# Kernel optimization log

Measured on AMD Instinct MI355X. Metric: run time of the kernel, lower is better.

Reference implementation:

```python
import jax, jax.numpy as jnp
import numpy as np

K = 128
NITER = 10


def _sq_dist(x, c):
    x2 = jnp.sum(x * x, axis=1, keepdims=True)          # [N,1]
    c2 = jnp.sum(c * c, axis=1)                          # [K]
    return x2 + c2[None, :] - 2.0 * (x @ c.T)


def _kmeans(x, key):
    N, D = x.shape
    idx = jax.random.permutation(key, N)[:K]             # torch.randperm(N)[:K]
    c0 = x[idx]

    def step(c, _):
        cl = jnp.argmin(_sq_dist(x, c), axis=1)          # nearest assignment [N]
        counts = jax.ops.segment_sum(jnp.ones((N,), x.dtype), cl, num_segments=K)  # bincount
        sums = jax.ops.segment_sum(x, cl, num_segments=K)                          # [K,D] (vectorized over D)
        # c = sums / counts; NaN (empty cluster, 0/0) -> 0, matching c[isnan(c)]=0
        c_new = jnp.where(counts[:, None] > 0, sums / jnp.maximum(counts, 1.0)[:, None], 0.0)
        return c_new, None

    c, _ = jax.lax.scan(step, c0, None, length=NITER)
    return c


def setup_inputs() -> dict:
    key = jax.random.key(0)
    x = jax.random.normal(key, (500000, 64), dtype=jnp.float32)
    return {"x": x}


def reference(x):
    # KMeans runs on x.detach(); forward output has no grad path through centroids
    centroids = _kmeans(jax.lax.stop_gradient(x), jax.random.key(42))
    distances = _sq_dist(x, centroids)                   # [N, K]
    # Faithful to normalize_distance: distances.sum(1, keepdim=True)[0] indexes
    # ROW 0 of the [N,1] row-sums -> a single scalar broadcast to all rows.
    denom = jnp.sum(distances[0])
    probs = 1.0 - distances / denom
    return probs
```

## Files before the change

kernel.cpp:

```cpp
#include <hip/hip_runtime.h>
#include <cstdint>
#include <cstddef>

#define NPTS 500000
#define DIM 64
#define KC 128
#define KM_ITERS 10
#define NGROUPS (NPTS / 32)
#define NITERS8 ((NGROUPS + 7) / 8)

typedef __bf16 bf16x8 __attribute__((ext_vector_type(8)));
typedef float f32x4 __attribute__((ext_vector_type(4)));

__device__ __forceinline__ float wave_reduce_add(float v) {
#pragma unroll
  for (int off = 32; off > 0; off >>= 1) v += __shfl_xor(v, off, 64);
  return v;
}

__device__ __forceinline__ bf16x8 cvt8(float4 a, float4 b) {
  bf16x8 r;
  r[0] = (__bf16)a.x; r[1] = (__bf16)a.y; r[2] = (__bf16)a.z; r[3] = (__bf16)a.w;
  r[4] = (__bf16)b.x; r[5] = (__bf16)b.y; r[6] = (__bf16)b.z; r[7] = (__bf16)b.w;
  return r;
}

__global__ void k_cvt(const float* __restrict__ x, bf16x8* __restrict__ xb8) {
  int n = NPTS * DIM / 8;
  for (int i = blockIdx.x * 256 + threadIdx.x; i < n; i += gridDim.x * 256) {
    const float4* xp = (const float4*)(x + (size_t)i * 8);
    xb8[i] = cvt8(xp[0], xp[1]);
  }
}

__global__ void k_initc(const float* __restrict__ x, float* __restrict__ cent,
                        float* __restrict__ c2, float* __restrict__ sums,
                        float* __restrict__ cnts) {
  int k = blockIdx.x, d = threadIdx.x;
  long src = (long)k * 3891 + 7;
  float v = x[src * DIM + d];
  cent[k * DIM + d] = v;
  sums[k * DIM + d] = 0.f;
  float s = wave_reduce_add(v * v);
  if (d == 0) { c2[k] = s; cnts[k] = 0.f; }
}

__global__ void k_update(const float* __restrict__ sums, const float* __restrict__ cnts,
                         float* __restrict__ cent, float* __restrict__ c2,
                         float* __restrict__ sums_z, float* __restrict__ cnts_z) {
  int k = blockIdx.x, d = threadIdx.x;
  float c = cnts[k];
  float v = (c > 0.f) ? (sums[k * DIM + d] / c) : 0.f;
  cent[k * DIM + d] = v;
  sums_z[k * DIM + d] = 0.f;
  float s = wave_reduce_add(v * v);
  if (d == 0) { c2[k] = s; cnts_z[k] = 0.f; }
}

#define DIST_H(V0, V1, MK)                                                     \
  {                                                                            \
    f32x4 acc_[8];                                                             \
    _Pragma("unroll") for (int tt = 0; tt < 8; tt++)                           \
      acc_[tt] = (f32x4){c2h[tt * 4 + 0], c2h[tt * 4 + 1],                     \
                         c2h[tt * 4 + 2], c2h[tt * 4 + 3]};                    \
    _Pragma("unroll") for (int tt = 0; tt < 8; tt++)                           \
      acc_[tt] = __builtin_amdgcn_mfma_f32_16x16x32_bf16(afr0[tt], V0, acc_[tt], 0, 0, 0); \
    _Pragma("unroll") for (int tt = 0; tt < 8; tt++)                           \
      acc_[tt] = __builtin_amdgcn_mfma_f32_16x16x32_bf16(afr1[tt], V1, acc_[tt], 0, 0, 0); \
    float tv[32]; int ti[32];                                                  \
    _Pragma("unroll") for (int i_ = 0; i_ < 32; i_++) {                        \
      tv[i_] = acc_[i_ >> 2][i_ & 3]; ti[i_] = i_;                             \
    }                                                                          \
    _Pragma("unroll") for (int s_ = 16; s_ >= 1; s_ >>= 1)                     \
      _Pragma("unroll") for (int i_ = 0; i_ < s_; i_++) {                      \
        bool t_ = tv[i_ + s_] > tv[i_];                                        \
        tv[i_] = t_ ? tv[i_ + s_] : tv[i_];                                    \
        ti[i_] = t_ ? ti[i_ + s_] : ti[i_];                                    \
      }                                                                        \
    float maxv = tv[0];                                                        \
    int mk = ((ti[0] >> 2) << 4) + grp * 4 + (ti[0] & 3);                      \
    _Pragma("unroll") for (int off = 16; off <= 32; off <<= 1) {               \
      float ov = __shfl_xor(maxv, off, 64);                                    \
      int ok = __shfl_xor(mk, off, 64);                                        \
      if (ov > maxv || (ov == maxv && ok < mk)) { maxv = ov; mk = ok; }        \
    }                                                                          \
    MK = mk;                                                                   \
  }

#define XT_WRITE(XTW, V0, V1, H)                                               \
  {                                                                            \
    int slotb = (((((H) << 1) | (col >> 3)) ^ grp) & 3) * 16 + (col & 7) * 2;  \
    _Pragma("unroll") for (int j = 0; j < 8; j++) {                            \
      *(__bf16*)((XTW) + (grp * 8 + j) * 80 + slotb) = V0[j];                  \
      *(__bf16*)((XTW) + (32 + grp * 8 + j) * 80 + slotb) = V1[j];             \
    }                                                                          \
  }

__global__ __launch_bounds__(256, 2)
void k_assign(const __bf16* __restrict__ xb, const float* __restrict__ cent,
              const float* __restrict__ c2, float* __restrict__ sums,
              float* __restrict__ cnts) {
  __shared__ char xT[8][5120];
  __shared__ int sm[8][32];
  __shared__ float lc[KC];

  const int lane = threadIdx.x & 63;
  const int wid = threadIdx.x >> 6;
  const int col = lane & 15;
  const int grp = lane >> 4;

  bf16x8 afr0[8], afr1[8];
  float c2h[32];
#pragma unroll
  for (int t = 0; t < 8; t++) {
    const float* cp = cent + (size_t)(t * 16 + col) * DIM;
    afr0[t] = cvt8(*(const float4*)(cp + grp * 8), *(const float4*)(cp + grp * 8 + 4));
    afr1[t] = cvt8(*(const float4*)(cp + 32 + grp * 8), *(const float4*)(cp + 32 + grp * 8 + 4));
#pragma unroll
    for (int r = 0; r < 4; r++) c2h[t * 4 + r] = -0.5f * c2[t * 16 + grp * 4 + r];
  }
#pragma unroll
  for (int t = 0; t < 8; t++) asm volatile("" : "+v"(afr0[t]), "+v"(afr1[t]));
#pragma unroll
  for (int i = 0; i < 32; i++) asm volatile("" : "+v"(c2h[i]));

  for (int i = threadIdx.x; i < KC; i += 256) lc[i] = 0.f;
  __syncthreads();

  f32x4 accs[8];
#pragma unroll
  for (int i = 0; i < 8; i++) accs[i] = (f32x4){0.f, 0.f, 0.f, 0.f};

  const int kbase = wid * 32;

  for (int it = blockIdx.x; it < NITERS8; it += gridDim.x) {
    int g0 = it * 8 + wid * 2, g1 = g0 + 1;
    bool e0 = g0 < NGROUPS, e1 = g1 < NGROUPS;

    bf16x8 v0a, v1a, v0b, v1b, w0a, w1a, w0b, w1b;
    if (e0) {
      const bf16x8* xr = (const bf16x8*)(xb + (size_t)(g0 * 32 + col) * DIM + grp * 8);
      v0a = xr[0]; v1a = xr[4]; v0b = xr[128]; v1b = xr[132];
    }
    if (e1) {
      const bf16x8* xr = (const bf16x8*)(xb + (size_t)(g1 * 32 + col) * DIM + grp * 8);
      w0a = xr[0]; w1a = xr[4]; w0b = xr[128]; w1b = xr[132];
    }

    int mk0a = -1, mk0b = -1, mk1a = -1, mk1b = -1;
    if (e0) {
      char* xTw = xT[wid * 2];
      XT_WRITE(xTw, v0a, v1a, 0);
      XT_WRITE(xTw, v0b, v1b, 1);
      DIST_H(v0a, v1a, mk0a);
      DIST_H(v0b, v1b, mk0b);
      if (grp == 0) { atomicAdd(&lc[mk0a], 1.f); atomicAdd(&lc[mk0b], 1.f); }
    }
    if (grp == 0) { sm[wid * 2][col] = mk0a; sm[wid * 2][16 + col] = mk0b; }
    if (e1) {
      char* xTw = xT[wid * 2 + 1];
      XT_WRITE(xTw, w0a, w1a, 0);
      XT_WRITE(xTw, w0b, w1b, 1);
      DIST_H(w0a, w1a, mk1a);
      DIST_H(w0b, w1b, mk1b);
      if (grp == 0) { atomicAdd(&lc[mk1a], 1.f); atomicAdd(&lc[mk1b], 1.f); }
    }
    if (grp == 0) { sm[wid * 2 + 1][col] = mk1a; sm[wid * 2 + 1][16 + col] = mk1b; }
    __syncthreads();

#pragma unroll
    for (int G = 0; G < 8; G++) {
      const int* smG = sm[G];
      int4 mlo = *(const int4*)&smG[grp * 8];
      int4 mhi = *(const int4*)&smG[grp * 8 + 4];
      const char* xTg = xT[G];
      bf16x8 xf0, xf1, xf2, xf3;
      { int d = col;      int s = (grp ^ ((d >> 3) & 3)) & 3; xf0 = *(const bf16x8*)(xTg + d * 80 + s * 16); }
      { int d = 16 + col; int s = (grp ^ ((d >> 3) & 3)) & 3; xf1 = *(const bf16x8*)(xTg + d * 80 + s * 16); }
      { int d = 32 + col; int s = (grp ^ ((d >> 3) & 3)) & 3; xf2 = *(const bf16x8*)(xTg + d * 80 + s * 16); }
      { int d = 48 + col; int s = (grp ^ ((d >> 3) & 3)) & 3; xf3 = *(const bf16x8*)(xTg + d * 80 + s * 16); }
      int m0 = mlo.x, m1 = mlo.y, m2 = mlo.z, m3 = mlo.w;
      int m4 = mhi.x, m5 = mhi.y, m6 = mhi.z, m7 = mhi.w;
#pragma unroll
      for (int tt2 = 0; tt2 < 2; tt2++) {
        int c = kbase + tt2 * 16 + col;
        union { unsigned u[4]; bf16x8 v; } oh;
        oh.u[0] = (m0 == c ? 0x3F80u : 0u) | (m1 == c ? 0x3F800000u : 0u);
        oh.u[1] = (m2 == c ? 0x3F80u : 0u) | (m3 == c ? 0x3F800000u : 0u);
        oh.u[2] = (m4 == c ? 0x3F80u : 0u) | (m5 == c ? 0x3F800000u : 0u);
        oh.u[3] = (m6 == c ? 0x3F80u : 0u) | (m7 == c ? 0x3F800000u : 0u);
        accs[tt2 * 4 + 0] = __builtin_amdgcn_mfma_f32_16x16x32_bf16(oh.v, xf0, accs[tt2 * 4 + 0], 0, 0, 0);
        accs[tt2 * 4 + 1] = __builtin_amdgcn_mfma_f32_16x16x32_bf16(oh.v, xf1, accs[tt2 * 4 + 1], 0, 0, 0);
        accs[tt2 * 4 + 2] = __builtin_amdgcn_mfma_f32_16x16x32_bf16(oh.v, xf2, accs[tt2 * 4 + 2], 0, 0, 0);
        accs[tt2 * 4 + 3] = __builtin_amdgcn_mfma_f32_16x16x32_bf16(oh.v, xf3, accs[tt2 * 4 + 3], 0, 0, 0);
      }
    }
    __syncthreads();
  }

#pragma unroll
  for (int tt2 = 0; tt2 < 2; tt2++)
#pragma unroll
    for (int dt = 0; dt < 4; dt++)
#pragma unroll
      for (int r = 0; r < 4; r++)
        atomicAdd(&sums[(size_t)(kbase + tt2 * 16 + grp * 4 + r) * DIM + dt * 16 + col],
                  accs[tt2 * 4 + dt][r]);
  for (int i = threadIdx.x; i < KC; i += 256) atomicAdd(&cnts[i], lc[i]);
}

__global__ __launch_bounds__(256, 2)
void k_probs(const float* __restrict__ x, const float* __restrict__ cent,
             const float* __restrict__ c2, float* __restrict__ out) {
  const int lane = threadIdx.x & 63;
  const int wid = threadIdx.x >> 6;
  const int col = lane & 15;
  const int grp = lane >> 4;

  bf16x8 afr[2][8];
  float c2g[32];
#pragma unroll
  for (int t = 0; t < 8; t++) {
    const float* cp = cent + (size_t)(t * 16 + col) * DIM;
#pragma unroll
    for (int ks = 0; ks < 2; ks++) {
      float4 f0 = *(const float4*)(cp + ks * 32 + grp * 8);
      float4 f1 = *(const float4*)(cp + ks * 32 + grp * 8 + 4);
      afr[ks][t] = cvt8(f0, f1);
    }
#pragma unroll
    for (int r = 0; r < 4; r++) c2g[t * 4 + r] = c2[t * 16 + grp * 4 + r];
  }

  float c2a = c2[lane], c2b = c2[64 + lane];
  float x2_0 = 0.f, dA = 0.f, dB = 0.f;
#pragma unroll 8
  for (int d = 0; d < DIM; d++) {
    float xv = x[d];
    x2_0 = fmaf(xv, xv, x2_0);
    dA = fmaf(xv, cent[(size_t)lane * DIM + d], dA);
    dB = fmaf(xv, cent[(size_t)(64 + lane) * DIM + d], dB);
  }
  float part = ((x2_0 + c2a) - 2.f * dA) + ((x2_0 + c2b) - 2.f * dB);
  float invd = 1.0f / wave_reduce_add(part);

  int w = blockIdx.x * 4 + wid;
  int nw = gridDim.x * 4;
  for (int t = w; t < NPTS / 16; t += nw) {
    int n0 = t * 16;
    const float* xp = x + (size_t)(n0 + col) * DIM;
    float4 a0 = *(const float4*)(xp + grp * 8);
    float4 a1 = *(const float4*)(xp + grp * 8 + 4);
    float4 b0 = *(const float4*)(xp + 32 + grp * 8);
    float4 b1 = *(const float4*)(xp + 32 + grp * 8 + 4);
    bf16x8 xb0 = cvt8(a0, a1), xb1 = cvt8(b0, b1);

    float sq = a0.x * a0.x + a0.y * a0.y + a0.z * a0.z + a0.w * a0.w
             + a1.x * a1.x + a1.y * a1.y + a1.z * a1.z + a1.w * a1.w
             + b0.x * b0.x + b0.y * b0.y + b0.z * b0.z + b0.w * b0.w
             + b1.x * b1.x + b1.y * b1.y + b1.z * b1.z + b1.w * b1.w;
    sq += __shfl_xor(sq, 16, 64);
    sq += __shfl_xor(sq, 32, 64);

    f32x4 acc[8];
#pragma unroll
    for (int tt = 0; tt < 8; tt++) acc[tt] = (f32x4){0.f, 0.f, 0.f, 0.f};
#pragma unroll
    for (int tt = 0; tt < 8; tt++)
      acc[tt] = __builtin_amdgcn_mfma_f32_16x16x32_bf16(afr[0][tt], xb0, acc[tt], 0, 0, 0);
#pragma unroll
    for (int tt = 0; tt < 8; tt++)
      acc[tt] = __builtin_amdgcn_mfma_f32_16x16x32_bf16(afr[1][tt], xb1, acc[tt], 0, 0, 0);

    float* op = out + (size_t)(n0 + col) * KC + grp * 4;
#pragma unroll
    for (int tt = 0; tt < 8; tt++) {
      float4 q;
      q.x = 1.f - ((sq + c2g[tt * 4 + 0]) - 2.f * acc[tt][0]) * invd;
      q.y = 1.f - ((sq + c2g[tt * 4 + 1]) - 2.f * acc[tt][1]) * invd;
      q.z = 1.f - ((sq + c2g[tt * 4 + 2]) - 2.f * acc[tt][2]) * invd;
      q.w = 1.f - ((sq + c2g[tt * 4 + 3]) - 2.f * acc[tt][3]) * invd;
      *(float4*)(op + tt * 16) = q;
    }
  }
}

extern "C" void kernel_launch(void* const* d_in, const int* in_sizes, int n_in,
                              void* d_out, int out_size, void* d_ws, size_t ws_size,
                              hipStream_t stream) {
  const float* x = (const float*)d_in[0];
  float* out = (float*)d_out;

  float* cent = (float*)d_ws;
  float* c2 = cent + KC * DIM;
  float* sums = c2 + KC;
  float* cnts = sums + KC * DIM;

  bf16x8* xb8 = (bf16x8*)d_out;
  const __bf16* xb = (const __bf16*)d_out;

  k_cvt<<<2048, 256, 0, stream>>>(x, xb8);
  k_initc<<<KC, DIM, 0, stream>>>(x, cent, c2, sums, cnts);
  for (int it = 0; it < KM_ITERS; it++) {
    k_assign<<<512, 256, 0, stream>>>(xb, cent, c2, sums, cnts);
    k_update<<<KC, DIM, 0, stream>>>(sums, cnts, cent, c2, sums, cnts);
  }
  k_probs<<<512, 256, 0, stream>>>(x, cent, c2, out);
}
```

Before: 713.6 us.

## Fuse bf16 conversion into first assign pass, prefetch next tile, nontemporal output stores

Result: faster. 675.0 us (-5.4%).

```diff
diff --git a/kernel.cpp b/kernel.cpp
--- a/kernel.cpp
+++ b/kernel.cpp
@@ -23,14 +23,6 @@
   r[0] = (__bf16)a.x; r[1] = (__bf16)a.y; r[2] = (__bf16)a.z; r[3] = (__bf16)a.w;
   r[4] = (__bf16)b.x; r[5] = (__bf16)b.y; r[6] = (__bf16)b.z; r[7] = (__bf16)b.w;
   return r;
-}
-
-__global__ void k_cvt(const float* __restrict__ x, bf16x8* __restrict__ xb8) {
-  int n = NPTS * DIM / 8;
-  for (int i = blockIdx.x * 256 + threadIdx.x; i < n; i += gridDim.x * 256) {
-    const float4* xp = (const float4*)(x + (size_t)i * 8);
-    xb8[i] = cvt8(xp[0], xp[1]);
-  }
 }
 
 __global__ void k_initc(const float* __restrict__ x, float* __restrict__ cent,
@@ -96,8 +88,10 @@
     }                                                                          \
   }
 
+template <int FIRST>
 __global__ __launch_bounds__(256, 2)
-void k_assign(const __bf16* __restrict__ xb, const float* __restrict__ cent,
+void k_assign(const float* __restrict__ xf, const __bf16* __restrict__ xb,
+              __bf16* __restrict__ xbw, const float* __restrict__ cent,
               const float* __restrict__ c2, float* __restrict__ sums,
               float* __restrict__ cnts) {
   __shared__ char xT[8][5120];
@@ -133,18 +127,47 @@
 
   const int kbase = wid * 32;
 
+  bf16x8 p0a, p1a, p0b, p1b;
+  if constexpr (!FIRST) {
+    int g0 = blockIdx.x * 8 + wid * 2;
+    if (blockIdx.x < NITERS8 && g0 < NGROUPS) {
+      const bf16x8* xr = (const bf16x8*)(xb + (size_t)(g0 * 32 + col) * DIM + grp * 8);
+      p0a = xr[0]; p1a = xr[4]; p0b = xr[128]; p1b = xr[132];
+    }
+  }
+
   for (int it = blockIdx.x; it < NITERS8; it += gridDim.x) {
     int g0 = it * 8 + wid * 2, g1 = g0 + 1;
     bool e0 = g0 < NGROUPS, e1 = g1 < NGROUPS;
 
     bf16x8 v0a, v1a, v0b, v1b, w0a, w1a, w0b, w1b;
-    if (e0) {
-      const bf16x8* xr = (const bf16x8*)(xb + (size_t)(g0 * 32 + col) * DIM + grp * 8);
-      v0a = xr[0]; v1a = xr[4]; v0b = xr[128]; v1b = xr[132];
-    }
-    if (e1) {
-      const bf16x8* xr = (const bf16x8*)(xb + (size_t)(g1 * 32 + col) * DIM + grp * 8);
-      w0a = xr[0]; w1a = xr[4]; w0b = xr[128]; w1b = xr[132];
+    if constexpr (FIRST) {
+      if (e0) {
+        const float* xp = xf + (size_t)(g0 * 32 + col) * DIM + grp * 8;
+        const float* xq = xp + 16 * DIM;
+        v0a = cvt8(*(const float4*)xp, *(const float4*)(xp + 4));
+        v1a = cvt8(*(const float4*)(xp + 32), *(const float4*)(xp + 36));
+        v0b = cvt8(*(const float4*)xq, *(const float4*)(xq + 4));
+        v1b = cvt8(*(const float4*)(xq + 32), *(const float4*)(xq + 36));
+        bf16x8* wp = (bf16x8*)(xbw + (size_t)(g0 * 32 + col) * DIM);
+        wp[grp] = v0a; wp[4 + grp] = v1a; wp[128 + grp] = v0b; wp[132 + grp] = v1b;
+      }
+      if (e1) {
+        const float* xp = xf + (size_t)(g1 * 32 + col) * DIM + grp * 8;
+        const float* xq = xp + 16 * DIM;
+        w0a = cvt8(*(const float4*)xp, *(const float4*)(xp + 4));
+        w1a = cvt8(*(const float4*)(xp + 32), *(const float4*)(xp + 36));
+        w0b = cvt8(*(const float4*)xq, *(const float4*)(xq + 4));
+        w1b = cvt8(*(const float4*)(xq + 32), *(const float4*)(xq + 36));
+        bf16x8* wp = (bf16x8*)(xbw + (size_t)(g1 * 32 + col) * DIM);
+        wp[grp] = w0a; wp[4 + grp] = w1a; wp[128 + grp] = w0b; wp[132 + grp] = w1b;
+      }
+    } else {
+      v0a = p0a; v1a = p1a; v0b = p0b; v1b = p1b;
+      if (e1) {
+        const bf16x8* xr = (const bf16x8*)(xb + (size_t)(g1 * 32 + col) * DIM + grp * 8);
+        w0a = xr[0]; w1a = xr[4]; w0b = xr[128]; w1b = xr[132];
+      }
     }
 
     int mk0a = -1, mk0b = -1, mk1a = -1, mk1b = -1;
@@ -167,6 +190,15 @@
     }
     if (grp == 0) { sm[wid * 2 + 1][col] = mk1a; sm[wid * 2 + 1][16 + col] = mk1b; }
     __syncthreads();
+
+    if constexpr (!FIRST) {
+      int itn = it + gridDim.x;
+      int g0n = itn * 8 + wid * 2;
+      if (itn < NITERS8 && g0n < NGROUPS) {
+        const bf16x8* xr = (const bf16x8*)(xb + (size_t)(g0n * 32 + col) * DIM + grp * 8);
+        p0a = xr[0]; p1a = xr[4]; p0b = xr[128]; p1b = xr[132];
+      }
+    }
 
 #pragma unroll
     for (int G = 0; G < 8; G++) {
@@ -275,12 +307,12 @@
     float* op = out + (size_t)(n0 + col) * KC + grp * 4;
 #pragma unroll
     for (int tt = 0; tt < 8; tt++) {
-      float4 q;
-      q.x = 1.f - ((sq + c2g[tt * 4 + 0]) - 2.f * acc[tt][0]) * invd;
-      q.y = 1.f - ((sq + c2g[tt * 4 + 1]) - 2.f * acc[tt][1]) * invd;
-      q.z = 1.f - ((sq + c2g[tt * 4 + 2]) - 2.f * acc[tt][2]) * invd;
-      q.w = 1.f - ((sq + c2g[tt * 4 + 3]) - 2.f * acc[tt][3]) * invd;
-      *(float4*)(op + tt * 16) = q;
+      f32x4 q;
+      q[0] = 1.f - ((sq + c2g[tt * 4 + 0]) - 2.f * acc[tt][0]) * invd;
+      q[1] = 1.f - ((sq + c2g[tt * 4 + 1]) - 2.f * acc[tt][1]) * invd;
+      q[2] = 1.f - ((sq + c2g[tt * 4 + 2]) - 2.f * acc[tt][2]) * invd;
+      q[3] = 1.f - ((sq + c2g[tt * 4 + 3]) - 2.f * acc[tt][3]) * invd;
+      __builtin_nontemporal_store(q, (f32x4*)(op + tt * 16));
     }
   }
 }
@@ -296,13 +328,13 @@
   float* sums = c2 + KC;
   float* cnts = sums + KC * DIM;
 
-  bf16x8* xb8 = (bf16x8*)d_out;
-  const __bf16* xb = (const __bf16*)d_out;
-
-  k_cvt<<<2048, 256, 0, stream>>>(x, xb8);
+  __bf16* xb = (__bf16*)d_out;
+
   k_initc<<<KC, DIM, 0, stream>>>(x, cent, c2, sums, cnts);
-  for (int it = 0; it < KM_ITERS; it++) {
-    k_assign<<<512, 256, 0, stream>>>(xb, cent, c2, sums, cnts);
+  k_assign<1><<<512, 256, 0, stream>>>(x, xb, xb, cent, c2, sums, cnts);
+  k_update<<<KC, DIM, 0, stream>>>(sums, cnts, cent, c2, sums, cnts);
+  for (int it = 1; it < KM_ITERS; it++) {
+    k_assign<0><<<512, 256, 0, stream>>>(x, xb, xb, cent, c2, sums, cnts);
     k_update<<<KC, DIM, 0, stream>>>(sums, cnts, cent, c2, sums, cnts);
   }
   k_probs<<<512, 256, 0, stream>>>(x, cent, c2, out);
```
